# Kernel optimization log

Measured on AMD Instinct MI355X. Metric: run time of the kernel, lower is better.

The kernel has to match this reference:

```python
import jax, jax.numpy as jnp
import numpy as np

NBITS = 1
GROUP_SIZE = 64
OUT_F = 4096
IN_F = 4096


def setup_inputs() -> dict:
    key = jax.random.key(0)
    k1, k2, k3, k4, k5 = jax.random.split(key, 5)
    x = jax.random.normal(k1, (8192, IN_F), dtype=jnp.float32)
    # packed 1-bit weights: 8 bits per byte, stored as int32 in [0,256)
    W_packed = jax.random.randint(k2, (OUT_F, IN_F // 8), 0, 256, dtype=jnp.int32)
    n_groups = OUT_F * IN_F // GROUP_SIZE
    scale = jax.random.uniform(k3, (n_groups, 1), dtype=jnp.float32) * 0.02 + 0.005
    zero = jax.random.normal(k4, (n_groups, 1), dtype=jnp.float32) * 0.5
    bias = jax.random.normal(k5, (OUT_F,), dtype=jnp.float32) * 0.02
    return {"x": x, "W_packed": W_packed, "scale": scale, "zero": zero, "bias": bias}


def _unpack_1bit(W_packed):
    # (out, in//8) int -> (out, in) float bits, bit 0 first within each byte
    bits = (W_packed[..., None] >> jnp.arange(8, dtype=jnp.int32)) & 1  # (out, in//8, 8)
    return bits.reshape(W_packed.shape[0], -1).astype(jnp.float32)      # (out, in)


def _dequantise(W_packed, scale, zero):
    W_q = _unpack_1bit(W_packed)                       # (out, in)
    W_grouped = W_q.reshape(-1, GROUP_SIZE)            # (n_groups, group_size), axis=1 grouping
    W_hat = (W_grouped - zero) * scale                 # per-group affine dequant
    return W_hat.reshape(OUT_F, IN_F)


def reference(x, W_packed, scale, zero, bias):
    W_hat = _dequantise(W_packed, scale, zero)
    # F.linear: x @ W_hat.T + bias
    return jnp.dot(x, W_hat.T) + bias
```

## Files before the change

kernel.cpp:

```cpp
#include <hip/hip_runtime.h>
#include <hip/hip_bf16.h>

#define IN_F   4096
#define OUT_F  4096
#define BK     64
#define NTILES (IN_F / BK)

typedef __bf16 bf16;
typedef __attribute__((ext_vector_type(8)))  __bf16 bf16x8;
typedef __attribute__((ext_vector_type(4)))  __bf16 bf16x4;
typedef __attribute__((ext_vector_type(4)))  float  floatx4;

__global__ __launch_bounds__(256) void prep_kernel(
    const float* __restrict__ x,  bf16* __restrict__ xb,
    const int* __restrict__ Wp,   const float* __restrict__ scale,
    const float* __restrict__ zero, bf16* __restrict__ Wb, int nxb)
{
    if ((int)blockIdx.x < nxb) {
        const size_t i = (size_t)blockIdx.x * 256 + threadIdx.x;
        const float4 v0 = ((const float4*)x)[2 * i];
        const float4 v1 = ((const float4*)x)[2 * i + 1];
        bf16x8 b;
        b[0] = (bf16)v0.x; b[1] = (bf16)v0.y; b[2] = (bf16)v0.z; b[3] = (bf16)v0.w;
        b[4] = (bf16)v1.x; b[5] = (bf16)v1.y; b[6] = (bf16)v1.z; b[7] = (bf16)v1.w;
        ((bf16x8*)xb)[i] = b;
    } else {
        const int tid = (blockIdx.x - nxb) * 256 + threadIdx.x;
        const int n = tid >> 9;
        const int b = tid & 511;
        const int g = (n << 6) + (b >> 3);
        const float sc = scale[g];
        const float zp = zero[g];
        const bf16 hi = (bf16)((1.0f - zp) * sc);
        const bf16 lo = (bf16)((0.0f - zp) * sc);
        const int v = Wp[tid];
        bf16x8 w;
#pragma unroll
        for (int j = 0; j < 8; ++j) w[j] = ((v >> j) & 1) ? hi : lo;
        *(bf16x8*)&Wb[(size_t)tid * 8] = w;
    }
}

__device__ __forceinline__ void gload_lds16(const void* g, void* l) {
    __builtin_amdgcn_global_load_lds(
        (const __attribute__((address_space(1))) unsigned int*)g,
        (__attribute__((address_space(3))) unsigned int*)l, 16, 0, 0);
}

#define CFENCE asm volatile("" ::: "memory")
#define SBAR() do { CFENCE; __builtin_amdgcn_s_barrier(); CFENCE; } while (0)
#define WAIT_LGKM0 asm volatile("s_waitcnt lgkmcnt(0)" ::: "memory")

#define STAGE(src, ldsTile, q, row0, kti) do {                                 \
    const int r_  = (q) * 64 + wave * 8 + srow;                                \
    const int gu_ = sun ^ (r_ & 7);                                            \
    gload_lds16((src) + (size_t)((row0) + r_) * IN_F + (kti) * BK + gu_ * 8,   \
                (ldsTile) + ((q) * 64 + wave * 8) * BK);                       \
} while (0)

#define LDFRAG(tile, row, u) \
    (*(const bf16x8*)((tile) + (row) * BK + (((u) ^ ((row) & 7)) << 3)))

#define LOAD_A(tile, MS)                                                       \
    _Pragma("unroll")                                                          \
    for (int i = 0; i < 4; ++i)                                                \
        _Pragma("unroll")                                                      \
        for (int ks = 0; ks < 2; ++ks)                                         \
            af[i][ks] = LDFRAG((tile), wm * 128 + (MS) * 64 + i * 16 + l15,    \
                               ks * 4 + l4);

#define LOAD_B_TO(dst, tile, NS)                                               \
    _Pragma("unroll")                                                          \
    for (int j = 0; j < 2; ++j)                                                \
        _Pragma("unroll")                                                      \
        for (int ks = 0; ks < 2; ++ks)                                         \
            dst[j][ks] = LDFRAG((tile), wn * 64 + (NS) * 32 + j * 16 + l15,    \
                                ks * 4 + l4);

#define MFMA_QUAD(AI, BJ, BFR)                                                 \
    __builtin_amdgcn_s_setprio(1);                                             \
    _Pragma("unroll")                                                          \
    for (int ks = 0; ks < 2; ++ks)                                             \
        _Pragma("unroll")                                                      \
        for (int i = 0; i < 4; ++i)                                            \
            _Pragma("unroll")                                                  \
            for (int j = 0; j < 2; ++j)                                        \
                acc[(AI) + i][(BJ) + j] =                                      \
                    __builtin_amdgcn_mfma_f32_16x16x32_bf16(                   \
                        af[i][ks], BFR[j][ks], acc[(AI) + i][(BJ) + j], 0, 0, 0); \
    __builtin_amdgcn_s_setprio(0);

__global__ __launch_bounds__(512, 2) void gemm256_8phase_kernel(
    const bf16* __restrict__ A,
    const bf16* __restrict__ B,
    const float* __restrict__ bias,
    float* __restrict__ out)
{
    __shared__ __align__(16) bf16 as_[2][256 * BK];
    __shared__ __align__(16) bf16 bs_[2][256 * BK];

    const int t    = threadIdx.x;
    const int lane = t & 63;
    const int wave = t >> 6;
    const int wm   = wave >> 2;
    const int wn   = wave & 3;
    const int l15  = lane & 15;
    const int l4   = lane >> 4;
    const int srow = lane >> 3;
    const int sun  = lane & 7;

    const int nwg = (int)gridDim.x;
    const int cpx = nwg >> 3;
    const int wg  = ((int)blockIdx.x & 7) * cpx + ((int)blockIdx.x >> 3);
    const int n0  = (wg & 15) * 256;
    const int m0  = (wg >> 4) * 256;

    floatx4 acc[8][4];
#pragma unroll
    for (int f = 0; f < 8; ++f)
#pragma unroll
        for (int g = 0; g < 4; ++g) acc[f][g] = (floatx4){0.f, 0.f, 0.f, 0.f};

#pragma unroll
    for (int q = 0; q < 4; ++q) STAGE(A, &as_[0][0], q, m0, 0);
#pragma unroll
    for (int q = 0; q < 4; ++q) STAGE(B, &bs_[0][0], q, n0, 0);
    STAGE(A, &as_[1][0], 0, m0, 1);
    STAGE(A, &as_[1][0], 2, m0, 1);
    asm volatile("s_waitcnt vmcnt(2)" ::: "memory");
    SBAR();

    bf16x8 af[4][2], bf0[2][2], bf1[2][2];

    for (int kt = 0; kt < NTILES; ++kt) {
        bf16* const At = &as_[kt & 1][0];
        bf16* const Bt = &bs_[kt & 1][0];
        bf16* const An = &as_[(kt & 1) ^ 1][0];
        bf16* const Bn = &bs_[(kt & 1) ^ 1][0];
        const int s1 = (kt + 1 < NTILES);
        const int s2 = (kt + 2 < NTILES);

        LOAD_A(At, 0);
        LOAD_B_TO(bf0, Bt, 0);
        if (s1) { STAGE(B, Bn, 0, n0, kt + 1); STAGE(B, Bn, 1, n0, kt + 1); }
        SBAR(); WAIT_LGKM0;
        MFMA_QUAD(0, 0, bf0);
        SBAR();

        LOAD_B_TO(bf1, Bt, 1);
        if (s1) { STAGE(B, Bn, 2, n0, kt + 1); STAGE(B, Bn, 3, n0, kt + 1); }
        SBAR(); WAIT_LGKM0;
        MFMA_QUAD(0, 2, bf1);
        if (s1) { asm volatile("s_waitcnt vmcnt(6)" ::: "memory"); }
        else    { asm volatile("s_waitcnt vmcnt(0)" ::: "memory"); }
        SBAR();

        LOAD_A(At, 1);
        if (s1) { STAGE(A, An, 1, m0, kt + 1); STAGE(A, An, 3, m0, kt + 1); }
        SBAR(); WAIT_LGKM0;
        MFMA_QUAD(4, 0, bf0);
        SBAR();

        if (s2) { STAGE(A, At, 0, m0, kt + 2); STAGE(A, At, 2, m0, kt + 2); }
        MFMA_QUAD(4, 2, bf1);
        if (s2) { asm volatile("s_waitcnt vmcnt(4)" ::: "memory"); }
        else    { asm volatile("s_waitcnt vmcnt(2)" ::: "memory"); }
        SBAR();
    }

#pragma unroll
    for (int g = 0; g < 4; ++g) {
        const int col = n0 + wn * 64 + g * 16 + l15;
        const float bv = bias[col];
#pragma unroll
        for (int f = 0; f < 8; ++f) {
            const int row = m0 + wm * 128 + f * 16 + l4 * 4;
#pragma unroll
            for (int r = 0; r < 4; ++r)
                out[(size_t)(row + r) * OUT_F + col] = acc[f][g][r] + bv;
        }
    }
}

#define SA 72
#define SB 72
__global__ __launch_bounds__(256) void hqq_gemm_fused_kernel(
    const float* __restrict__ x, const int* __restrict__ Wp,
    const float* __restrict__ scale, const float* __restrict__ zero,
    const float* __restrict__ bias, float* __restrict__ out)
{
    __shared__ __align__(16) bf16 asmem[128 * SA];
    __shared__ __align__(16) bf16 bsmem[128 * SB];
    const int t = threadIdx.x, lane = t & 63, wave = t >> 6;
    const int lane16 = lane & 15, kq = lane >> 4;
    const int wm = wave >> 1, wn = wave & 1;
    const int n0 = blockIdx.x * 128, m0 = blockIdx.y * 128;
    floatx4 acc[4][4];
#pragma unroll
    for (int i = 0; i < 4; ++i)
#pragma unroll
        for (int j = 0; j < 4; ++j) acc[i][j] = (floatx4){0.f, 0.f, 0.f, 0.f};
    const int a_col4 = t & 15, a_row0 = t >> 4;
    const int b_nl = t >> 1, b_half = t & 1;
    for (int kt = 0; kt < IN_F / 64; ++kt) {
        const float* xp = x + (size_t)(m0 + a_row0) * IN_F + kt * 64 + a_col4 * 4;
#pragma unroll
        for (int p = 0; p < 8; ++p) {
            float4 v = *(const float4*)(xp + (size_t)(p * 16) * IN_F);
            bf16x4 b = { (bf16)v.x, (bf16)v.y, (bf16)v.z, (bf16)v.w };
            *(bf16x4*)&asmem[(a_row0 + p * 16) * SA + a_col4 * 4] = b;
        }
        {
            const int4 v = *(const int4*)(Wp + (size_t)(n0 + b_nl) * (IN_F / 8)
                                          + kt * 8 + b_half * 4);
            const int g = (n0 + b_nl) * (IN_F / 64) + kt;
            const float sc = scale[g], zp = zero[g];
            const bf16 hi = (bf16)((1.0f - zp) * sc), lo = (bf16)(0.0f - zp * sc);
            const int vals[4] = {v.x, v.y, v.z, v.w};
#pragma unroll
            for (int e = 0; e < 4; ++e) {
                bf16x8 w;
#pragma unroll
                for (int j = 0; j < 8; ++j) w[j] = ((vals[e] >> j) & 1) ? hi : lo;
                *(bf16x8*)&bsmem[b_nl * SB + b_half * 32 + e * 8] = w;
            }
        }
        __syncthreads();
#pragma unroll
        for (int ks = 0; ks < 2; ++ks) {
            bf16x8 af[4], bfr[4];
#pragma unroll
            for (int i = 0; i < 4; ++i)
                af[i] = *(const bf16x8*)&asmem[(wm * 64 + i * 16 + lane16) * SA + ks * 32 + kq * 8];
#pragma unroll
            for (int j = 0; j < 4; ++j)
                bfr[j] = *(const bf16x8*)&bsmem[(wn * 64 + j * 16 + lane16) * SB + ks * 32 + kq * 8];
#pragma unroll
            for (int i = 0; i < 4; ++i)
#pragma unroll
                for (int j = 0; j < 4; ++j)
                    acc[i][j] = __builtin_amdgcn_mfma_f32_16x16x32_bf16(af[i], bfr[j], acc[i][j], 0, 0, 0);
        }
        __syncthreads();
    }
#pragma unroll
    for (int j = 0; j < 4; ++j) {
        const int col = n0 + wn * 64 + j * 16 + lane16;
        const float bv = bias[col];
#pragma unroll
        for (int i = 0; i < 4; ++i) {
            const int row = m0 + wm * 64 + i * 16 + kq * 4;
#pragma unroll
            for (int r = 0; r < 4; ++r)
                out[(size_t)(row + r) * OUT_F + col] = acc[i][j][r] + bv;
        }
    }
}

extern "C" void kernel_launch(void* const* d_in, const int* in_sizes, int n_in,
                              void* d_out, int out_size, void* d_ws, size_t ws_size,
                              hipStream_t stream) {
    const float* x     = (const float*)d_in[0];
    const int*   Wp    = (const int*)d_in[1];
    const float* scale = (const float*)d_in[2];
    const float* zero  = (const float*)d_in[3];
    const float* bias  = (const float*)d_in[4];
    float*       out   = (float*)d_out;

    const int M = in_sizes[0] / IN_F;
    const size_t need = (size_t)M * IN_F * 2 + (size_t)OUT_F * IN_F * 2;

    if (ws_size >= need && (M % 256) == 0) {
        bf16* xb = (bf16*)d_ws;
        bf16* Wb = (bf16*)((char*)d_ws + (size_t)M * IN_F * 2);

        const int nxb = (M * IN_F / 8) / 256;
        const int nwb = (OUT_F * IN_F / 8) / 256;
        prep_kernel<<<nxb + nwb, 256, 0, stream>>>(x, xb, Wp, scale, zero, Wb, nxb);

        gemm256_8phase_kernel<<<dim3((OUT_F / 256) * (M / 256)), 512, 0, stream>>>(
            xb, Wb, bias, out);
    } else {
        dim3 grid(OUT_F / 128, M / 128);
        hqq_gemm_fused_kernel<<<grid, 256, 0, stream>>>(x, Wp, scale, zero, bias, out);
    }
}
```

Measured before the change: 476.0 us.

## Restructure GEMM main loop into fewer phases with double A-fragment registers

The 8-phase main loop is collapsed into fewer barrier-separated phases. Both B fragment sets are loaded up front, and a second A fragment buffer (afn) lets the second half of A be loaded while the first MFMAs run. The explicit lgkmcnt(0) waits are replaced by sched_barrier hints, and the vmcnt thresholds are adjusted to match. Separately, the x-to-bf16 conversion in the prep kernel now handles 4 elements per thread instead of 8, doubling its block count. This adds register pressure, and the removed LDS waits depend on the compiler inserting the right waitcnt before the MFMAs.

Result: no change. 482.0 us (+1.3%).

```diff
diff --git a/kernel.cpp b/kernel.cpp
--- a/kernel.cpp
+++ b/kernel.cpp
@@ -18,12 +18,9 @@
 {
     if ((int)blockIdx.x < nxb) {
         const size_t i = (size_t)blockIdx.x * 256 + threadIdx.x;
-        const float4 v0 = ((const float4*)x)[2 * i];
-        const float4 v1 = ((const float4*)x)[2 * i + 1];
-        bf16x8 b;
-        b[0] = (bf16)v0.x; b[1] = (bf16)v0.y; b[2] = (bf16)v0.z; b[3] = (bf16)v0.w;
-        b[4] = (bf16)v1.x; b[5] = (bf16)v1.y; b[6] = (bf16)v1.z; b[7] = (bf16)v1.w;
-        ((bf16x8*)xb)[i] = b;
+        float4 v = ((const float4*)x)[i];
+        bf16x4 b = { (bf16)v.x, (bf16)v.y, (bf16)v.z, (bf16)v.w };
+        ((bf16x4*)xb)[i] = b;
     } else {
         const int tid = (blockIdx.x - nxb) * 256 + threadIdx.x;
         const int n = tid >> 9;
@@ -49,7 +46,7 @@
 
 #define CFENCE asm volatile("" ::: "memory")
 #define SBAR() do { CFENCE; __builtin_amdgcn_s_barrier(); CFENCE; } while (0)
-#define WAIT_LGKM0 asm volatile("s_waitcnt lgkmcnt(0)" ::: "memory")
+#define SCHED0 __builtin_amdgcn_sched_barrier(0)
 
 #define STAGE(src, ldsTile, q, row0, kti) do {                                 \
     const int r_  = (q) * 64 + wave * 8 + srow;                                \
@@ -61,13 +58,13 @@
 #define LDFRAG(tile, row, u) \
     (*(const bf16x8*)((tile) + (row) * BK + (((u) ^ ((row) & 7)) << 3)))
 
-#define LOAD_A(tile, MS)                                                       \
+#define LOAD_A_TO(dst, tile, MS)                                               \
     _Pragma("unroll")                                                          \
     for (int i = 0; i < 4; ++i)                                                \
         _Pragma("unroll")                                                      \
         for (int ks = 0; ks < 2; ++ks)                                         \
-            af[i][ks] = LDFRAG((tile), wm * 128 + (MS) * 64 + i * 16 + l15,    \
-                               ks * 4 + l4);
+            dst[i][ks] = LDFRAG((tile), wm * 128 + (MS) * 64 + i * 16 + l15,   \
+                                ks * 4 + l4);
 
 #define LOAD_B_TO(dst, tile, NS)                                               \
     _Pragma("unroll")                                                          \
@@ -77,7 +74,7 @@
             dst[j][ks] = LDFRAG((tile), wn * 64 + (NS) * 32 + j * 16 + l15,    \
                                 ks * 4 + l4);
 
-#define MFMA_QUAD(AI, BJ, BFR)                                                 \
+#define MFMA_QUAD(AI, BJ, AF, BFR)                                             \
     __builtin_amdgcn_s_setprio(1);                                             \
     _Pragma("unroll")                                                          \
     for (int ks = 0; ks < 2; ++ks)                                             \
@@ -87,7 +84,7 @@
             for (int j = 0; j < 2; ++j)                                        \
                 acc[(AI) + i][(BJ) + j] =                                      \
                     __builtin_amdgcn_mfma_f32_16x16x32_bf16(                   \
-                        af[i][ks], BFR[j][ks], acc[(AI) + i][(BJ) + j], 0, 0, 0); \
+                        AF[i][ks], BFR[j][ks], acc[(AI) + i][(BJ) + j], 0, 0, 0); \
     __builtin_amdgcn_s_setprio(0);
 
 __global__ __launch_bounds__(512, 2) void gemm256_8phase_kernel(
@@ -130,7 +127,7 @@
     asm volatile("s_waitcnt vmcnt(2)" ::: "memory");
     SBAR();
 
-    bf16x8 af[4][2], bf0[2][2], bf1[2][2];
+    bf16x8 af[4][2], afn[4][2], bf0[2][2], bf1[2][2];
 
     for (int kt = 0; kt < NTILES; ++kt) {
         bf16* const At = &as_[kt & 1][0];
@@ -140,29 +137,27 @@
         const int s1 = (kt + 1 < NTILES);
         const int s2 = (kt + 2 < NTILES);
 
-        LOAD_A(At, 0);
+        LOAD_A_TO(af, At, 0);
         LOAD_B_TO(bf0, Bt, 0);
         if (s1) { STAGE(B, Bn, 0, n0, kt + 1); STAGE(B, Bn, 1, n0, kt + 1); }
-        SBAR(); WAIT_LGKM0;
-        MFMA_QUAD(0, 0, bf0);
-        SBAR();
-
         LOAD_B_TO(bf1, Bt, 1);
-        if (s1) { STAGE(B, Bn, 2, n0, kt + 1); STAGE(B, Bn, 3, n0, kt + 1); }
-        SBAR(); WAIT_LGKM0;
-        MFMA_QUAD(0, 2, bf1);
-        if (s1) { asm volatile("s_waitcnt vmcnt(6)" ::: "memory"); }
+        SCHED0;
+        MFMA_QUAD(0, 0, af, bf0);
+        if (s1) { asm volatile("s_waitcnt vmcnt(4)" ::: "memory"); }
         else    { asm volatile("s_waitcnt vmcnt(0)" ::: "memory"); }
         SBAR();
 
-        LOAD_A(At, 1);
+        LOAD_A_TO(afn, At, 1);
+        if (s1) { STAGE(B, Bn, 2, n0, kt + 1); STAGE(B, Bn, 3, n0, kt + 1); }
+        SCHED0;
+        MFMA_QUAD(0, 2, af, bf1);
+        SBAR();
+
         if (s1) { STAGE(A, An, 1, m0, kt + 1); STAGE(A, An, 3, m0, kt + 1); }
-        SBAR(); WAIT_LGKM0;
-        MFMA_QUAD(4, 0, bf0);
-        SBAR();
-
         if (s2) { STAGE(A, At, 0, m0, kt + 2); STAGE(A, At, 2, m0, kt + 2); }
-        MFMA_QUAD(4, 2, bf1);
+        SCHED0;
+        MFMA_QUAD(4, 0, afn, bf0);
+        MFMA_QUAD(4, 2, afn, bf1);
         if (s2) { asm volatile("s_waitcnt vmcnt(4)" ::: "memory"); }
         else    { asm volatile("s_waitcnt vmcnt(2)" ::: "memory"); }
         SBAR();
@@ -274,7 +269,7 @@
         bf16* xb = (bf16*)d_ws;
         bf16* Wb = (bf16*)((char*)d_ws + (size_t)M * IN_F * 2);
 
-        const int nxb = (M * IN_F / 8) / 256;
+        const int nxb = (M * IN_F / 4) / 256;
         const int nwb = (OUT_F * IN_F / 8) / 256;
         prep_kernel<<<nxb + nwb, 256, 0, stream>>>(x, xb, Wp, scale, zero, Wb, nxb);
 
```
